# Kernel optimization log

Measured on AMD Instinct MI355X. Metric: run time of the kernel, lower is better.

The kernel has to match this reference:

```python
import jax, jax.numpy as jnp
import numpy as np

HIDDEN = 768
NUM_HEADS = 12
HEAD_DIM = HIDDEN // NUM_HEADS  # 64
ROPE_BASE = 10000.0


def _rope_cos_sin(position_ids, dim=HEAD_DIM, base=ROPE_BASE):
    # matches ModernBERTRotaryEmbedding: freqs [B,S,dim/2], emb = cat(freqs,freqs)
    inv_freq = 1.0 / (base ** (jnp.arange(0, dim, 2, dtype=jnp.float32) / dim))
    freqs = position_ids.astype(jnp.float32)[:, :, None] * inv_freq[None, None, :]
    emb = jnp.concatenate([freqs, freqs], axis=-1)  # [B, S, dim]
    return jnp.cos(emb), jnp.sin(emb)


def _apply_rope(q, k, cos, sin):
    # q,k: [B, H, S, D]; cos,sin: [B, S, D]
    cos_half = cos[:, None, :, 0::2]  # [B,1,S,D/2]
    sin_half = sin[:, None, :, 0::2]
    def rot(x):
        xe, xo = x[..., 0::2], x[..., 1::2]
        re = xe * cos_half - xo * sin_half
        ro = xo * cos_half + xe * sin_half
        return jnp.stack([re, ro], axis=-1).reshape(x.shape)  # interleave back
    return rot(q), rot(k)


def setup_inputs() -> dict:
    key = jax.random.key(0)
    k1, k2, k3 = jax.random.split(key, 3)
    B, S = 2, 2048
    hidden_states = jax.random.normal(k1, (B, S, HIDDEN), dtype=jnp.float32)
    position_ids = jnp.broadcast_to(jnp.arange(S, dtype=jnp.int64 if jax.config.jax_enable_x64 else jnp.int32)[None, :], (B, S))
    # torch nn.Linear weights: [out_features, in_features]
    Wqkv = jax.random.normal(k2, (3 * HIDDEN, HIDDEN), dtype=jnp.float32) * (HIDDEN ** -0.5)
    Wo = jax.random.normal(k3, (HIDDEN, HIDDEN), dtype=jnp.float32) * (HIDDEN ** -0.5)
    return {"hidden_states": hidden_states, "Wqkv": Wqkv, "Wo": Wo, "position_ids": position_ids}


def reference(hidden_states, Wqkv, Wo, position_ids):
    B, S, _ = hidden_states.shape
    qkv = hidden_states @ Wqkv.T  # [B, S, 3H]
    qkv = qkv.reshape(B, S, 3, NUM_HEADS, HEAD_DIM).transpose(2, 0, 3, 1, 4)
    q, k, v = qkv[0], qkv[1], qkv[2]  # [B, H, S, D]
    cos, sin = _rope_cos_sin(position_ids)
    q, k = _apply_rope(q, k, cos, sin)
    q = q * (HEAD_DIM ** -0.5)
    scores = jnp.einsum('bhqd,bhkd->bhqk', q, k)
    probs = jax.nn.softmax(scores, axis=-1)
    ctx = jnp.einsum('bhqk,bhkd->bhqd', probs, v)
    ctx = ctx.transpose(0, 2, 1, 3).reshape(B, S, HIDDEN)
    return ctx @ Wo.T
```

## Files before the change

### kernel.cpp

```cpp
#include <hip/hip_runtime.h>
#include <hip/hip_bf16.h>

typedef unsigned short u16;
typedef unsigned int u32;
typedef __attribute__((ext_vector_type(4))) float f32x4;
typedef __attribute__((ext_vector_type(8))) short short8;
typedef __attribute__((ext_vector_type(4))) short short4v;
typedef __attribute__((ext_vector_type(2))) unsigned int u32x2;

typedef const __attribute__((address_space(1))) unsigned int gu32;
typedef __attribute__((address_space(3))) unsigned int lu32;

__device__ __forceinline__ u16 f2b(float f) {
  unsigned u = __float_as_uint(f);
  u += 0x7fffu + ((u >> 16) & 1u);
  return (u16)(u >> 16);
}
__device__ __forceinline__ float b2f(u16 v) {
  return __uint_as_float(((unsigned)v) << 16);
}

__global__ __launch_bounds__(256) void cvt_kernel(const float* __restrict__ s0, u16* __restrict__ d0, int n0,
                                                  const float* __restrict__ s1, u16* __restrict__ d1, int n1,
                                                  const float* __restrict__ s2, u16* __restrict__ d2, int n2) {
  const int total = n0 + n1 + n2;
  for (int i = blockIdx.x * 256 + threadIdx.x; i < total; i += gridDim.x * 256) {
    const float* s; u16* d; int j = i;
    if (j < n0)            { s = s0; d = d0; }
    else if ((j -= n0) < n1) { s = s1; d = d1; }
    else                   { j -= n1; s = s2; d = d2; }
    f32x4 v = reinterpret_cast<const f32x4*>(s)[j];
    short4v o;
    for (int t = 0; t < 4; ++t) o[t] = (short)f2b(v[t]);
    reinterpret_cast<short4v*>(d)[j] = o;
  }
}

template<int BM, int NFR, int EPI>
__global__ __launch_bounds__(256) void gemm_bf(const u16* __restrict__ A,
                                               const u16* __restrict__ B,
                                               void* __restrict__ Cp,
                                               const int* __restrict__ pos,
                                               u16* __restrict__ Qo, u16* __restrict__ Ko,
                                               u16* __restrict__ VTo,
                                               int M, int N, int K) {
  constexpr int BN = NFR * 32;
  constexpr int MFR = BM / 32;
  __shared__ alignas(128) char smem[BM * 64 + BN * 64];
  char* AsB = smem;
  char* BsB = smem + BM * 64;

  const int tid = threadIdx.x;
  const int lane = tid & 63;
  const int wv = tid >> 6;
  const int wr = wv >> 1, wc = wv & 1;
  const int bm = blockIdx.y * BM, bn = blockIdx.x * BN;
  const int ro = lane & 15, qu = lane >> 4;

  const int arow = tid >> 2;
  const int abyte = ((tid & 3) * 16) ^ ((arow & 3) << 4);
  const size_t K2 = (size_t)K * 2;

  f32x4 acc[MFR][NFR] = {};

  for (int kk = 0; kk < K; kk += 32) {
    const char* aptr = (const char*)(A + (size_t)(bm + arow) * K + kk) + abyte;
    const char* bptr = (const char*)(B + (size_t)(bn + arow) * K + kk) + abyte;
    char* adst = AsB + wv * 1024;
    char* bdst = BsB + wv * 1024;
    __builtin_amdgcn_global_load_lds((gu32*)aptr, (lu32*)adst, 16, 0, 0);
    if constexpr (BM == 128)
      __builtin_amdgcn_global_load_lds((gu32*)(aptr + 64 * K2), (lu32*)(adst + 4096), 16, 0, 0);
    __builtin_amdgcn_global_load_lds((gu32*)bptr, (lu32*)bdst, 16, 0, 0);
    if constexpr (NFR == 4) {
      __builtin_amdgcn_global_load_lds((gu32*)(bptr + 64 * K2), (lu32*)(bdst + 4096), 16, 0, 0);
    } else if constexpr (NFR == 3) {
      if (wv < 2)
        __builtin_amdgcn_global_load_lds((gu32*)(bptr + 64 * K2), (lu32*)(BsB + 4096 + wv * 1024), 16, 0, 0);
    }
    __syncthreads();

    short8 af[MFR], bfr[NFR];
    for (int m = 0; m < MFR; ++m) {
      const int r = wr * (BM / 2) + m * 16 + ro;
      af[m] = *reinterpret_cast<const short8*>(AsB + r * 64 + ((qu * 16) ^ ((r & 3) << 4)));
    }
    for (int n = 0; n < NFR; ++n) {
      const int r = wc * (NFR * 16) + n * 16 + ro;
      bfr[n] = *reinterpret_cast<const short8*>(BsB + r * 64 + ((qu * 16) ^ ((r & 3) << 4)));
    }
    for (int m = 0; m < MFR; ++m)
      for (int n = 0; n < NFR; ++n)
        acc[m][n] = __builtin_amdgcn_mfma_f32_16x16x32_bf16(af[m], bfr[n], acc[m][n], 0, 0, 0);
    __syncthreads();
  }

  if constexpr (EPI != 2) {
    for (int m = 0; m < MFR; ++m)
      for (int n = 0; n < NFR; ++n)
        for (int r = 0; r < 4; ++r) {
          const int row = bm + wr * (BM / 2) + m * 16 + qu * 4 + r;
          const int col = bn + wc * (NFR * 16) + n * 16 + ro;
          if constexpr (EPI == 1) ((float*)Cp)[(size_t)row * N + col] = acc[m][n][r];
          else                    ((u16*)Cp)[(size_t)row * N + col] = f2b(acc[m][n][r]);
        }
  } else {
    const int sec = bn >= 1536 ? 2 : (bn >= 768 ? 1 : 0);
    const int colbase = bn + wc * (NFR * 16) - sec * 768;
    if (sec == 2) {
      for (int m = 0; m < MFR; ++m) {
        const int token = bm + wr * (BM / 2) + m * 16 + qu * 4;
        const int b = token >> 11, s = token & 2047;
        for (int n = 0; n < NFR; ++n) {
          const int col = colbase + n * 16 + ro;
          const int h = col >> 6, hd = col & 63;
          short4v o4;
          for (int r = 0; r < 4; ++r) o4[r] = (short)f2b(acc[m][n][r]);
          *reinterpret_cast<short4v*>(VTo + ((size_t)(b * 12 + h) * 64 + hd) * 2048 + s) = o4;
        }
      }
    } else {
      u16* Dst = sec ? Ko : Qo;
      const float scale = sec ? 1.0f : 0.125f;
      float invf[NFR];
      for (int n = 0; n < NFR; ++n) {
        const int mfreq = (colbase + n * 16 + ro) & 30;
        invf[n] = exp2f(-(float)mfreq * 0.41524101186092029f);
      }
      for (int m = 0; m < MFR; ++m)
        for (int r = 0; r < 4; ++r) {
          const int token = bm + wr * (BM / 2) + m * 16 + qu * 4 + r;
          const int b = token >> 11, s = token & 2047;
          const int p = pos[b * 2048 + s];
          for (int n = 0; n < NFR; ++n) {
            const int col = colbase + n * 16 + ro;
            const int h = col >> 6, hd = col & 63;
            const float v = acc[m][n][r];
            const float vp = __shfl_xor(v, 1);
            float sn, cs;
            __sincosf((float)p * invf[n], &sn, &cs);
            const float out = (hd & 1) ? (v * cs + vp * sn) : (v * cs - vp * sn);
            Dst[((size_t)(b * 12 + h) * 2048 + s) * 64 + hd] = f2b(out * scale);
          }
        }
    }
  }
}

__global__ __launch_bounds__(256) void attn_kernel(const u16* __restrict__ Q,
                                                   const u16* __restrict__ K,
                                                   const u16* __restrict__ VT,
                                                   u16* __restrict__ ctx) {
  __shared__ alignas(128) char smem[40960];

  const int tid = threadIdx.x;
  const int lane = tid & 63;
  const int wv = tid >> 6;
  const int bh = blockIdx.y;
  const int qbase = blockIdx.x * 64 + wv * 16;
  const int ro = lane & 15, qu = lane >> 4;

  const char* Kbh = (const char*)(K  + (size_t)bh * 2048 * 64);
  const char* Vbh = (const char*)(VT + (size_t)bh * 64 * 2048);
  char* P_base = smem + 32768 + wv * 2048;

  const int rlo  = tid >> 3;
  const int scol = ((tid & 7) * 16) ^ ((rlo & 7) << 4);

  const size_t qoff = ((size_t)bh * 2048 + qbase + ro) * 64 + qu * 8;
  short8 qf0 = *reinterpret_cast<const short8*>(Q + qoff);
  short8 qf1 = *reinterpret_cast<const short8*>(Q + qoff + 32);

  f32x4 o[4] = {};
  f32x4 lsumv = {};

  {
    char* db = smem + wv * 1024;
    __builtin_amdgcn_global_load_lds((gu32*)(Kbh + (size_t)rlo * 128 + scol),         (lu32*)(db), 16, 0, 0);
    __builtin_amdgcn_global_load_lds((gu32*)(Kbh + (size_t)(32 + rlo) * 128 + scol),  (lu32*)(db + 4096), 16, 0, 0);
    __builtin_amdgcn_global_load_lds((gu32*)(Vbh + (size_t)rlo * 4096 + scol),        (lu32*)(db + 8192), 16, 0, 0);
    __builtin_amdgcn_global_load_lds((gu32*)(Vbh + (size_t)(32 + rlo) * 4096 + scol), (lu32*)(db + 12288), 16, 0, 0);
  }
  __syncthreads();

  int cur = 0;
  for (int t = 0; t < 32; ++t) {
    if (t < 31) {
      const int kv = (t + 1) * 64;
      char* db = smem + (cur ^ 1) * 16384 + wv * 1024;
      __builtin_amdgcn_global_load_lds((gu32*)(Kbh + (size_t)(kv + rlo) * 128 + scol),           (lu32*)(db), 16, 0, 0);
      __builtin_amdgcn_global_load_lds((gu32*)(Kbh + (size_t)(kv + 32 + rlo) * 128 + scol),      (lu32*)(db + 4096), 16, 0, 0);
      __builtin_amdgcn_global_load_lds((gu32*)(Vbh + (size_t)rlo * 4096 + kv * 2 + scol),        (lu32*)(db + 8192), 16, 0, 0);
      __builtin_amdgcn_global_load_lds((gu32*)(Vbh + (size_t)(32 + rlo) * 4096 + kv * 2 + scol), (lu32*)(db + 12288), 16, 0, 0);
    }

    const char* kbuf = smem + cur * 16384;
    const char* vbuf = kbuf + 8192;

    f32x4 s[4] = {};
    for (int g = 0; g < 4; ++g) {
      const int r = g * 16 + ro;
      const int sw = (r & 7) << 4;
      const char* krow = kbuf + r * 128;
      short8 kf0 = *reinterpret_cast<const short8*>(krow + ((qu * 16) ^ sw));
      short8 kf1 = *reinterpret_cast<const short8*>(krow + ((64 + qu * 16) ^ sw));
      s[g] = __builtin_amdgcn_mfma_f32_16x16x32_bf16(kf0, qf0, s[g], 0, 0, 0);
      s[g] = __builtin_amdgcn_mfma_f32_16x16x32_bf16(kf1, qf1, s[g], 0, 0, 0);
    }

    f32x4 e[4];
    for (int g = 0; g < 4; ++g)
      for (int r = 0; r < 4; ++r)
        e[g][r] = __expf(s[g][r]);
    lsumv += (e[0] + e[1]) + (e[2] + e[3]);

    const int swp = (ro & 7) << 4;
    char* prow = P_base + ro * 128;
    for (int g = 0; g < 4; ++g) {
      u32 lo, hi;
      asm("v_cvt_pk_bf16_f32 %0, %1, %2" : "=v"(lo) : "v"(e[g][0]), "v"(e[g][1]));
      asm("v_cvt_pk_bf16_f32 %0, %1, %2" : "=v"(hi) : "v"(e[g][2]), "v"(e[g][3]));
      u32x2 pk; pk[0] = lo; pk[1] = hi;
      *reinterpret_cast<u32x2*>(prow + ((g * 32 + qu * 8) ^ swp)) = pk;
    }
    asm volatile("" ::: "memory");

    short8 pa0 = *reinterpret_cast<const short8*>(prow + ((qu * 16) ^ swp));
    short8 pa1 = *reinterpret_cast<const short8*>(prow + ((64 + qu * 16) ^ swp));

    for (int g = 0; g < 4; ++g) {
      const int r = g * 16 + ro;
      const int sw = (r & 7) << 4;
      const char* vrow = vbuf + r * 128;
      short8 vf0 = *reinterpret_cast<const short8*>(vrow + ((qu * 16) ^ sw));
      short8 vf1 = *reinterpret_cast<const short8*>(vrow + ((64 + qu * 16) ^ sw));
      o[g] = __builtin_amdgcn_mfma_f32_16x16x32_bf16(pa0, vf0, o[g], 0, 0, 0);
      o[g] = __builtin_amdgcn_mfma_f32_16x16x32_bf16(pa1, vf1, o[g], 0, 0, 0);
    }

    __syncthreads();
    cur ^= 1;
  }

  float l = (lsumv[0] + lsumv[1]) + (lsumv[2] + lsumv[3]);
  l += __shfl_xor(l, 16);
  l += __shfl_xor(l, 32);
  const float inv = 1.0f / l;
  float invr[4];
  for (int r = 0; r < 4; ++r) invr[r] = __shfl(inv, qu * 4 + r);

  const int b = bh / 12, h = bh % 12;
  for (int g = 0; g < 4; ++g)
    for (int r = 0; r < 4; ++r) {
      const int s_tok = qbase + qu * 4 + r;
      const size_t oi = ((size_t)b * 2048 + s_tok) * 768 + h * 64 + g * 16 + ro;
      ctx[oi] = f2b(o[g][r] * invr[r]);
    }
}

extern "C" void kernel_launch(void* const* d_in, const int* in_sizes, int n_in,
                              void* d_out, int out_size, void* d_ws, size_t ws_size,
                              hipStream_t stream) {
  const float* hidden = (const float*)d_in[0];
  const float* Wqkv   = (const float*)d_in[1];
  const float* Wo     = (const float*)d_in[2];
  const int*   pos    = (const int*)d_in[3];

  char* ws = (char*)d_ws;
  u16* A_bf  = (u16*)(ws);
  u16* Bq_bf = (u16*)(ws + 6291456);
  u16* Bo_bf = (u16*)(ws + 9830400);
  u16* Qb    = (u16*)(ws + 11010048);
  u16* Kb    = (u16*)(ws + 17301504);
  u16* VT    = (u16*)(ws + 23592960);
  u16* ctx   = (u16*)(ws + 29884416);

  cvt_kernel<<<2048, 256, 0, stream>>>(hidden, A_bf, 786432,
                                       Wqkv, Bq_bf, 442368,
                                       Wo, Bo_bf, 147456);
  gemm_bf<128, 3, 2><<<dim3(24, 32), 256, 0, stream>>>(A_bf, Bq_bf, nullptr, pos,
                                                       Qb, Kb, VT, 4096, 2304, 768);
  attn_kernel<<<dim3(32, 24), 256, 0, stream>>>(Qb, Kb, VT, ctx);
  gemm_bf<64, 3, 1><<<dim3(8, 64), 256, 0, stream>>>(ctx, Bo_bf, (void*)d_out, nullptr,
                                                     nullptr, nullptr, nullptr, 4096, 768, 768);
}
```

Measured before the change: 95.78 us.

## Process two query sub-tiles per wave in attention to reuse K/V fragments

The attention kernel now runs 2 waves (128 threads) per block instead of 4, with each wave handling 32 query rows as two 16-row sub-tiles. Each K and V fragment read from LDS feeds two MFMAs, which halves LDS fragment reads per MFMA. Each thread now issues twice as many async global-to-LDS loads per tile. The costs are more registers per wave and fewer waves per block for hiding latency, while the grid and LDS footprint stay the same.

```diff
diff --git a/kernel.cpp b/kernel.cpp
--- a/kernel.cpp
+++ b/kernel.cpp
@@ -147,7 +147,7 @@
   }
 }
 
-__global__ __launch_bounds__(256) void attn_kernel(const u16* __restrict__ Q,
+__global__ __launch_bounds__(128) void attn_kernel(const u16* __restrict__ Q,
                                                    const u16* __restrict__ K,
                                                    const u16* __restrict__ VT,
                                                    u16* __restrict__ ctx) {
@@ -157,76 +157,84 @@
   const int lane = tid & 63;
   const int wv = tid >> 6;
   const int bh = blockIdx.y;
-  const int qbase = blockIdx.x * 64 + wv * 16;
+  const int qbase = blockIdx.x * 64 + wv * 32;
   const int ro = lane & 15, qu = lane >> 4;
 
   const char* Kbh = (const char*)(K  + (size_t)bh * 2048 * 64);
   const char* Vbh = (const char*)(VT + (size_t)bh * 64 * 2048);
-  char* P_base = smem + 32768 + wv * 2048;
-
-  const int rlo  = tid >> 3;
-  const int scol = ((tid & 7) * 16) ^ ((rlo & 7) << 4);
-
-  const size_t qoff = ((size_t)bh * 2048 + qbase + ro) * 64 + qu * 8;
-  short8 qf0 = *reinterpret_cast<const short8*>(Q + qoff);
-  short8 qf1 = *reinterpret_cast<const short8*>(Q + qoff + 32);
-
-  f32x4 o[4] = {};
-  f32x4 lsumv = {};
-
-  {
-    char* db = smem + wv * 1024;
-    __builtin_amdgcn_global_load_lds((gu32*)(Kbh + (size_t)rlo * 128 + scol),         (lu32*)(db), 16, 0, 0);
-    __builtin_amdgcn_global_load_lds((gu32*)(Kbh + (size_t)(32 + rlo) * 128 + scol),  (lu32*)(db + 4096), 16, 0, 0);
-    __builtin_amdgcn_global_load_lds((gu32*)(Vbh + (size_t)rlo * 4096 + scol),        (lu32*)(db + 8192), 16, 0, 0);
-    __builtin_amdgcn_global_load_lds((gu32*)(Vbh + (size_t)(32 + rlo) * 4096 + scol), (lu32*)(db + 12288), 16, 0, 0);
-  }
+  char* P_base = smem + 32768 + wv * 4096;
+
+  const int sr = lane >> 3;
+  const int sc = ((lane & 7) * 16) ^ (sr << 4);
+  const int srow = 8 * wv + sr;
+
+  const size_t qoffA = ((size_t)bh * 2048 + qbase + ro) * 64 + qu * 8;
+  short8 qfA0 = *reinterpret_cast<const short8*>(Q + qoffA);
+  short8 qfA1 = *reinterpret_cast<const short8*>(Q + qoffA + 32);
+  short8 qfB0 = *reinterpret_cast<const short8*>(Q + qoffA + 16 * 64);
+  short8 qfB1 = *reinterpret_cast<const short8*>(Q + qoffA + 16 * 64 + 32);
+
+  f32x4 oA[4] = {}, oB[4] = {};
+  f32x4 lsumA = {}, lsumB = {};
+
+#define STAGE_TILE(db, kv)                                                                                      \
+  do {                                                                                                          \
+    __builtin_amdgcn_global_load_lds((gu32*)(Kbh + (size_t)((kv) + srow) * 128 + sc),      (lu32*)((db) + wv * 1024), 16, 0, 0);         \
+    __builtin_amdgcn_global_load_lds((gu32*)(Kbh + (size_t)((kv) + srow + 16) * 128 + sc), (lu32*)((db) + wv * 1024 + 2048), 16, 0, 0);  \
+    __builtin_amdgcn_global_load_lds((gu32*)(Kbh + (size_t)((kv) + srow + 32) * 128 + sc), (lu32*)((db) + 4096 + wv * 1024), 16, 0, 0);  \
+    __builtin_amdgcn_global_load_lds((gu32*)(Kbh + (size_t)((kv) + srow + 48) * 128 + sc), (lu32*)((db) + 4096 + wv * 1024 + 2048), 16, 0, 0); \
+    __builtin_amdgcn_global_load_lds((gu32*)(Vbh + (size_t)(srow) * 4096 + (kv) * 2 + sc),      (lu32*)((db) + 8192 + wv * 1024), 16, 0, 0);        \
+    __builtin_amdgcn_global_load_lds((gu32*)(Vbh + (size_t)(srow + 16) * 4096 + (kv) * 2 + sc), (lu32*)((db) + 8192 + wv * 1024 + 2048), 16, 0, 0); \
+    __builtin_amdgcn_global_load_lds((gu32*)(Vbh + (size_t)(srow + 32) * 4096 + (kv) * 2 + sc), (lu32*)((db) + 12288 + wv * 1024), 16, 0, 0);       \
+    __builtin_amdgcn_global_load_lds((gu32*)(Vbh + (size_t)(srow + 48) * 4096 + (kv) * 2 + sc), (lu32*)((db) + 12288 + wv * 1024 + 2048), 16, 0, 0);\
+  } while (0)
+
+  STAGE_TILE(smem, 0);
   __syncthreads();
 
   int cur = 0;
   for (int t = 0; t < 32; ++t) {
-    if (t < 31) {
-      const int kv = (t + 1) * 64;
-      char* db = smem + (cur ^ 1) * 16384 + wv * 1024;
-      __builtin_amdgcn_global_load_lds((gu32*)(Kbh + (size_t)(kv + rlo) * 128 + scol),           (lu32*)(db), 16, 0, 0);
-      __builtin_amdgcn_global_load_lds((gu32*)(Kbh + (size_t)(kv + 32 + rlo) * 128 + scol),      (lu32*)(db + 4096), 16, 0, 0);
-      __builtin_amdgcn_global_load_lds((gu32*)(Vbh + (size_t)rlo * 4096 + kv * 2 + scol),        (lu32*)(db + 8192), 16, 0, 0);
-      __builtin_amdgcn_global_load_lds((gu32*)(Vbh + (size_t)(32 + rlo) * 4096 + kv * 2 + scol), (lu32*)(db + 12288), 16, 0, 0);
-    }
+    if (t < 31) STAGE_TILE(smem + (cur ^ 1) * 16384, (t + 1) * 64);
 
     const char* kbuf = smem + cur * 16384;
     const char* vbuf = kbuf + 8192;
 
-    f32x4 s[4] = {};
+    f32x4 sA[4] = {}, sB[4] = {};
     for (int g = 0; g < 4; ++g) {
       const int r = g * 16 + ro;
       const int sw = (r & 7) << 4;
       const char* krow = kbuf + r * 128;
       short8 kf0 = *reinterpret_cast<const short8*>(krow + ((qu * 16) ^ sw));
       short8 kf1 = *reinterpret_cast<const short8*>(krow + ((64 + qu * 16) ^ sw));
-      s[g] = __builtin_amdgcn_mfma_f32_16x16x32_bf16(kf0, qf0, s[g], 0, 0, 0);
-      s[g] = __builtin_amdgcn_mfma_f32_16x16x32_bf16(kf1, qf1, s[g], 0, 0, 0);
-    }
-
-    f32x4 e[4];
-    for (int g = 0; g < 4; ++g)
-      for (int r = 0; r < 4; ++r)
-        e[g][r] = __expf(s[g][r]);
-    lsumv += (e[0] + e[1]) + (e[2] + e[3]);
+      sA[g] = __builtin_amdgcn_mfma_f32_16x16x32_bf16(kf0, qfA0, sA[g], 0, 0, 0);
+      sA[g] = __builtin_amdgcn_mfma_f32_16x16x32_bf16(kf1, qfA1, sA[g], 0, 0, 0);
+      sB[g] = __builtin_amdgcn_mfma_f32_16x16x32_bf16(kf0, qfB0, sB[g], 0, 0, 0);
+      sB[g] = __builtin_amdgcn_mfma_f32_16x16x32_bf16(kf1, qfB1, sB[g], 0, 0, 0);
+    }
 
     const int swp = (ro & 7) << 4;
-    char* prow = P_base + ro * 128;
+    char* prowA = P_base + ro * 128;
+    char* prowB = P_base + 2048 + ro * 128;
     for (int g = 0; g < 4; ++g) {
+      f32x4 eA, eB;
+      for (int r = 0; r < 4; ++r) { eA[r] = __expf(sA[g][r]); eB[r] = __expf(sB[g][r]); }
+      lsumA += eA; lsumB += eB;
       u32 lo, hi;
-      asm("v_cvt_pk_bf16_f32 %0, %1, %2" : "=v"(lo) : "v"(e[g][0]), "v"(e[g][1]));
-      asm("v_cvt_pk_bf16_f32 %0, %1, %2" : "=v"(hi) : "v"(e[g][2]), "v"(e[g][3]));
-      u32x2 pk; pk[0] = lo; pk[1] = hi;
-      *reinterpret_cast<u32x2*>(prow + ((g * 32 + qu * 8) ^ swp)) = pk;
+      asm("v_cvt_pk_bf16_f32 %0, %1, %2" : "=v"(lo) : "v"(eA[0]), "v"(eA[1]));
+      asm("v_cvt_pk_bf16_f32 %0, %1, %2" : "=v"(hi) : "v"(eA[2]), "v"(eA[3]));
+      u32x2 pkA; pkA[0] = lo; pkA[1] = hi;
+      *reinterpret_cast<u32x2*>(prowA + ((g * 32 + qu * 8) ^ swp)) = pkA;
+      asm("v_cvt_pk_bf16_f32 %0, %1, %2" : "=v"(lo) : "v"(eB[0]), "v"(eB[1]));
+      asm("v_cvt_pk_bf16_f32 %0, %1, %2" : "=v"(hi) : "v"(eB[2]), "v"(eB[3]));
+      u32x2 pkB; pkB[0] = lo; pkB[1] = hi;
+      *reinterpret_cast<u32x2*>(prowB + ((g * 32 + qu * 8) ^ swp)) = pkB;
     }
     asm volatile("" ::: "memory");
 
-    short8 pa0 = *reinterpret_cast<const short8*>(prow + ((qu * 16) ^ swp));
-    short8 pa1 = *reinterpret_cast<const short8*>(prow + ((64 + qu * 16) ^ swp));
+    short8 paA0 = *reinterpret_cast<const short8*>(prowA + ((qu * 16) ^ swp));
+    short8 paA1 = *reinterpret_cast<const short8*>(prowA + ((64 + qu * 16) ^ swp));
+    short8 paB0 = *reinterpret_cast<const short8*>(prowB + ((qu * 16) ^ swp));
+    short8 paB1 = *reinterpret_cast<const short8*>(prowB + ((64 + qu * 16) ^ swp));
 
     for (int g = 0; g < 4; ++g) {
       const int r = g * 16 + ro;
@@ -234,28 +242,46 @@
       const char* vrow = vbuf + r * 128;
       short8 vf0 = *reinterpret_cast<const short8*>(vrow + ((qu * 16) ^ sw));
       short8 vf1 = *reinterpret_cast<const short8*>(vrow + ((64 + qu * 16) ^ sw));
-      o[g] = __builtin_amdgcn_mfma_f32_16x16x32_bf16(pa0, vf0, o[g], 0, 0, 0);
-      o[g] = __builtin_amdgcn_mfma_f32_16x16x32_bf16(pa1, vf1, o[g], 0, 0, 0);
+      oA[g] = __builtin_amdgcn_mfma_f32_16x16x32_bf16(paA0, vf0, oA[g], 0, 0, 0);
+      oA[g] = __builtin_amdgcn_mfma_f32_16x16x32_bf16(paA1, vf1, oA[g], 0, 0, 0);
+      oB[g] = __builtin_amdgcn_mfma_f32_16x16x32_bf16(paB0, vf0, oB[g], 0, 0, 0);
+      oB[g] = __builtin_amdgcn_mfma_f32_16x16x32_bf16(paB1, vf1, oB[g], 0, 0, 0);
     }
 
     __syncthreads();
     cur ^= 1;
   }
-
-  float l = (lsumv[0] + lsumv[1]) + (lsumv[2] + lsumv[3]);
-  l += __shfl_xor(l, 16);
-  l += __shfl_xor(l, 32);
-  const float inv = 1.0f / l;
-  float invr[4];
-  for (int r = 0; r < 4; ++r) invr[r] = __shfl(inv, qu * 4 + r);
+#undef STAGE_TILE
 
   const int b = bh / 12, h = bh % 12;
-  for (int g = 0; g < 4; ++g)
-    for (int r = 0; r < 4; ++r) {
-      const int s_tok = qbase + qu * 4 + r;
-      const size_t oi = ((size_t)b * 2048 + s_tok) * 768 + h * 64 + g * 16 + ro;
-      ctx[oi] = f2b(o[g][r] * invr[r]);
-    }
+  {
+    float l = (lsumA[0] + lsumA[1]) + (lsumA[2] + lsumA[3]);
+    l += __shfl_xor(l, 16);
+    l += __shfl_xor(l, 32);
+    const float inv = 1.0f / l;
+    float invr[4];
+    for (int r = 0; r < 4; ++r) invr[r] = __shfl(inv, qu * 4 + r);
+    for (int g = 0; g < 4; ++g)
+      for (int r = 0; r < 4; ++r) {
+        const int s_tok = qbase + qu * 4 + r;
+        const size_t oi = ((size_t)b * 2048 + s_tok) * 768 + h * 64 + g * 16 + ro;
+        ctx[oi] = f2b(oA[g][r] * invr[r]);
+      }
+  }
+  {
+    float l = (lsumB[0] + lsumB[1]) + (lsumB[2] + lsumB[3]);
+    l += __shfl_xor(l, 16);
+    l += __shfl_xor(l, 32);
+    const float inv = 1.0f / l;
+    float invr[4];
+    for (int r = 0; r < 4; ++r) invr[r] = __shfl(inv, qu * 4 + r);
+    for (int g = 0; g < 4; ++g)
+      for (int r = 0; r < 4; ++r) {
+        const int s_tok = qbase + 16 + qu * 4 + r;
+        const size_t oi = ((size_t)b * 2048 + s_tok) * 768 + h * 64 + g * 16 + ro;
+        ctx[oi] = f2b(oB[g][r] * invr[r]);
+      }
+  }
 }
 
 extern "C" void kernel_launch(void* const* d_in, const int* in_sizes, int n_in,
@@ -280,7 +306,7 @@
                                        Wo, Bo_bf, 147456);
   gemm_bf<128, 3, 2><<<dim3(24, 32), 256, 0, stream>>>(A_bf, Bq_bf, nullptr, pos,
                                                        Qb, Kb, VT, 4096, 2304, 768);
-  attn_kernel<<<dim3(32, 24), 256, 0, stream>>>(Qb, Kb, VT, ctx);
+  attn_kernel<<<dim3(32, 24), 128, 0, stream>>>(Qb, Kb, VT, ctx);
   gemm_bf<64, 3, 1><<<dim3(8, 64), 256, 0, stream>>>(ctx, Bo_bf, (void*)d_out, nullptr,
                                                      nullptr, nullptr, nullptr, 4096, 768, 768);
 }
```

After: 102.1 us. +6.6%, slower.
